# Kernel optimization log

Hardware: AMD Instinct MI355X
Metric: run time of the kernel (lower is better)

Reference implementation:

```python
import jax, jax.numpy as jnp
import numpy as np

NUM_EXPERTS = 8


def setup_inputs() -> dict:
    key = jax.random.key(0)
    k1, k2, k3 = jax.random.split(key, 3)
    M, K, E, N, TOPK = 16384, 1024, NUM_EXPERTS, 2048, 2
    local_hidden_states = jax.random.normal(k1, (M, K), dtype=jnp.float32)
    up_weight = jax.random.normal(k2, (E, K, N), dtype=jnp.float32) * 0.02
    full_topk_ids = jax.random.randint(k3, (M, TOPK), 0, E, dtype=jnp.int64)
    return {
        "local_hidden_states": local_hidden_states,
        "up_weight": up_weight,
        "full_topk_ids": full_topk_ids,
    }


def reference(local_hidden_states, up_weight, full_topk_ids):
    # WORLD_SIZE == 1 -> all-gather is the identity; full token set == local shard.
    full_hidden = local_hidden_states                     # [M, K]
    M, K = full_hidden.shape
    E, _, N = up_weight.shape
    topk = full_topk_ids.shape[1]

    # Each token is routed to `topk` experts: replicate rows, flatten routing ids.
    h_rep = jnp.repeat(full_hidden, topk, axis=0)         # [M*topk, K]
    flat_ids = full_topk_ids.reshape(-1)                  # [M*topk]

    # Expert-grouped GEMM: out[p] = h_rep[p] @ up_weight[flat_ids[p]].
    # Loop over the small fixed expert count, masking rows (dense reference
    # for the irregular grouped GEMM; avoids a [M*topk, K, N] weight gather).
    inter = jnp.zeros((M * topk, N), dtype=full_hidden.dtype)
    for e in range(E):
        mask = (flat_ids == e).astype(full_hidden.dtype)[:, None]   # [M*topk, 1]
        inter = inter + (h_rep @ up_weight[e]) * mask                # [M*topk, N]

    # Fused gated SiLU: split the fused gate/up projection in half.
    half = N // 2
    gate, up = inter[:, :half], inter[:, half:]
    return jax.nn.silu(gate) * up                          # [M*topk, N//2]
```

## Files before the change

kernel.cpp:

```cpp
#include <hip/hip_runtime.h>
#include <hip/hip_bf16.h>
#include <stdint.h>

typedef __attribute__((ext_vector_type(4))) float f32x4;
typedef __attribute__((ext_vector_type(8))) short bf16x8;
typedef __attribute__((ext_vector_type(4))) float float4v;

static constexpr int KD    = 1024;
static constexpr int ND    = 2048;
static constexpr int NE    = 8;
static constexpr int MROWS = 16384;
static constexpr int RFLAT = 32768;
static constexpr int OUTN  = 1024;

static constexpr size_t WS_ROWLIST = 1024;
static constexpr size_t WS_HB      = 262144;
static constexpr size_t WS_WT      = 262144 + (size_t)33554432;

__device__ __forceinline__ unsigned short f2bf(float f) {
  uint32_t u = __float_as_uint(f);
  uint32_t r = (u + 0x7FFFu + ((u >> 16) & 1u)) >> 16;
  return (unsigned short)r;
}

__device__ __forceinline__ void gload16(const void* g, void* l) {
  __builtin_amdgcn_global_load_lds(
      (__attribute__((address_space(1))) void*)(void*)g,
      (__attribute__((address_space(3))) void*)l, 16, 0, 0);
}

__global__ void k_detect(const int* __restrict__ ids32, int* __restrict__ wsi) {
  int t = blockIdx.x * 256 + threadIdx.x;
  int i = 2 * t + 1;
  if (i < RFLAT && ids32[i] != 0) atomicOr(&wsi[31], 1);
}

__device__ __forceinline__ int read_id(const int* ids32, int t, int mode) {
  return (mode ? ids32[t] : ids32[2 * t]) & 7;
}

__global__ void k_count(const int* __restrict__ ids, int* __restrict__ wsi) {
  __shared__ int h[8];
  const int tid = threadIdx.x;
  if (tid < 8) h[tid] = 0;
  __syncthreads();
  const int mode = wsi[31];
  const int base = blockIdx.x * 512 + tid;
  atomicAdd(&h[read_id(ids, base, mode)], 1);
  atomicAdd(&h[read_id(ids, base + 256, mode)], 1);
  __syncthreads();
  if (tid < 8 && h[tid]) atomicAdd(&wsi[tid], h[tid]);
}

__global__ void k_scan(int* wsi) {
  if (threadIdx.x == 0) {
    int o = 0, to = 0;
    for (int e = 0; e < NE; ++e) {
      int c = wsi[e];
      wsi[16 + e] = o;
      wsi[8 + e]  = o;
      wsi[40 + e] = to;
      o += c;
      to += (c + 255) / 256;
    }
    wsi[16 + NE] = o;
    wsi[40 + NE] = to;
  }
}

__global__ void k_scatter(const int* __restrict__ ids, int* __restrict__ wsi,
                          int* __restrict__ rowlist) {
  __shared__ int h[8], base[8], c2[8];
  const int tid = threadIdx.x;
  if (tid < 8) { h[tid] = 0; c2[tid] = 0; }
  __syncthreads();
  const int mode = wsi[31];
  const int t = blockIdx.x * 256 + tid;
  const int e = read_id(ids, t, mode);
  atomicAdd(&h[e], 1);
  __syncthreads();
  if (tid < 8 && h[tid]) base[tid] = atomicAdd(&wsi[8 + tid], h[tid]);
  __syncthreads();
  const int r = atomicAdd(&c2[e], 1);
  rowlist[base[e] + r] = t;
}

__global__ void k_cvtH(const float* __restrict__ H, unsigned short* __restrict__ Hb) {
  const int n4 = (MROWS * KD) / 4;
  const int stride = gridDim.x * blockDim.x;
  for (int i = blockIdx.x * blockDim.x + threadIdx.x; i < n4; i += stride) {
    float4v v = ((const float4v*)H)[i];
    ushort4 o;
    o.x = f2bf(v.x); o.y = f2bf(v.y); o.z = f2bf(v.z); o.w = f2bf(v.w);
    ((ushort4*)Hb)[i] = o;
  }
}

__global__ void k_cvtW(const float* __restrict__ W, unsigned short* __restrict__ Wt) {
  __shared__ float tile[64][65];
  const int e  = blockIdx.z;
  const int n0 = blockIdx.x * 64;
  const int k0 = blockIdx.y * 64;
  const int tx = threadIdx.x, ty = threadIdx.y;
  const float* Wp = W + (size_t)e * KD * ND;
  #pragma unroll
  for (int i = ty; i < 64; i += 8)
    tile[i][tx] = Wp[(size_t)(k0 + i) * ND + n0 + tx];
  __syncthreads();
  unsigned short* Wo = Wt + (size_t)e * ND * KD;
  #pragma unroll
  for (int i = ty; i < 64; i += 8)
    Wo[(size_t)(n0 + i) * KD + k0 + tx] = f2bf(tile[tx][i]);
}

__global__ __launch_bounds__(512, 2) void k_gemm(
    const unsigned short* __restrict__ Hb, const unsigned short* __restrict__ Wt,
    const int* __restrict__ wsi, const int* __restrict__ rowlist,
    float* __restrict__ Out) {
  const int bid = blockIdx.x;
  const int xcd = bid & 7;
  const int j   = bid >> 3;
  const int colblk = j & 7;
  const int rt  = xcd + (j >> 3) * 8;
  if (rt >= wsi[48]) return;
  int e = 0;
  #pragma unroll
  for (int q = 1; q < 8; ++q)
    if (rt >= wsi[40 + q]) e = q;
  const int cnt = wsi[e];
  const int tile_base = (rt - wsi[40 + e]) * 256;
  const int tile_cnt = min(256, cnt - tile_base);
  const int off = wsi[16 + e] + tile_base;
  const int c0 = colblk * 128;

  __shared__ char lds[131072];
  __shared__ int s_rows[256];

  const int t = threadIdx.x;
  if (t < 256) s_rows[t] = rowlist[off + min(t, tile_cnt - 1)];
  __syncthreads();

  const int srow = t >> 2;
  const int coff = ((t & 3) ^ ((t >> 3) & 3)) * 16;
  const char* sA0 = (const char*)Hb + (size_t)(s_rows[srow] >> 1) * (KD * 2) + coff;
  const char* sA1 = (const char*)Hb + (size_t)(s_rows[128 + srow] >> 1) * (KD * 2) + coff;
  auto wcol_of = [&](int jc) {
    const int wn_s = jc >> 6, r64 = jc & 63;
    const int h_s = r64 >> 4, l_s = r64 & 15;
    return (h_s < 2) ? (c0 + wn_s * 32 + h_s * 16 + l_s)
                     : (OUTN + c0 + wn_s * 32 + (h_s - 2) * 16 + l_s);
  };
  const char* sB0 = (const char*)Wt + ((size_t)e * ND + wcol_of(srow)) * (KD * 2) + coff;
  const char* sB1 = (const char*)Wt + ((size_t)e * ND + wcol_of(128 + srow)) * (KD * 2) + coff;

  const int lane = t & 63, wid = t >> 6;
  const int wm = wid >> 2, wn = wid & 3;
  const int kc = lane >> 4, l15 = lane & 15;

  f32x4 acc[8][4];
  #pragma unroll
  for (int m = 0; m < 8; ++m)
    #pragma unroll
    for (int h = 0; h < 4; ++h)
      acc[m][h] = (f32x4){0.f, 0.f, 0.f, 0.f};

  int aoff[8], boff[4];
  #pragma unroll
  for (int m = 0; m < 8; ++m) {
    const int r = wm * 128 + m * 16 + l15;
    aoff[m] = r * 64 + ((kc ^ ((r >> 1) & 3)) * 16);
  }
  #pragma unroll
  for (int h = 0; h < 4; ++h) {
    const int jc = wn * 64 + h * 16 + l15;
    boff[h] = 16384 + jc * 64 + ((kc ^ ((jc >> 1) & 3)) * 16);
  }

  auto SAB = [&](int h, char* slot) {
    const int go = h * 64;
    gload16(sA0 + go, slot + t * 16);
    gload16(sA1 + go, slot + 8192 + t * 16);
    gload16(sB0 + go, slot + 16384 + t * 16);
    gload16(sB1 + go, slot + 24576 + t * 16);
  };

  bf16x8 af[4], bfv[4];
  auto LDA = [&](const char* cb, int mlo) {
    #pragma unroll
    for (int m = 0; m < 4; ++m) af[m] = *(const bf16x8*)(cb + aoff[mlo + m]);
  };
  auto LDB = [&](const char* cb) {
    #pragma unroll
    for (int h = 0; h < 4; ++h) bfv[h] = *(const bf16x8*)(cb + boff[h]);
  };
  auto MM = [&](int mlo) {
    __builtin_amdgcn_s_setprio(1);
    #pragma unroll
    for (int m = 0; m < 4; ++m)
      #pragma unroll
      for (int h = 0; h < 4; ++h)
        acc[mlo + m][h] =
            __builtin_amdgcn_mfma_f32_16x16x32_bf16(af[m], bfv[h], acc[mlo + m][h], 0, 0, 0);
    __builtin_amdgcn_s_setprio(0);
  };
#define GUARD8 asm volatile("s_waitcnt vmcnt(8)" ::: "memory")
#define GUARD4 asm volatile("s_waitcnt vmcnt(4)" ::: "memory")
#define GUARD0 asm volatile("s_waitcnt vmcnt(0)" ::: "memory")
#define BAR __builtin_amdgcn_s_barrier()

  SAB(0, lds);
  SAB(1, lds + 32768);
  SAB(2, lds + 65536);
  GUARD8; BAR;

  for (int k = 0; k < 14; ++k) {
    char* cb0 = lds + (k & 1) * 65536;
    char* cb1 = cb0 + 32768;
    char* st1 = lds + ((k + 1) & 1) * 65536 + 32768;
    LDA(cb0, 0); LDB(cb0);
    SAB(2 * k + 3, st1);
    BAR; MM(0); BAR;
    LDA(cb0, 4);
    GUARD8; BAR; MM(4); BAR;
    LDA(cb1, 0); LDB(cb1);
    SAB(2 * k + 4, cb0);
    BAR; MM(0); BAR;
    LDA(cb1, 4);
    GUARD8; BAR; MM(4); BAR;
  }
  {
    char* cb0 = lds;
    char* cb1 = lds + 32768;
    char* st1 = lds + 98304;
    LDA(cb0, 0); LDB(cb0);
    SAB(31, st1);
    BAR; MM(0); BAR;
    LDA(cb0, 4);
    GUARD8; BAR; MM(4); BAR;
    LDA(cb1, 0); LDB(cb1);
    BAR; MM(0); BAR;
    LDA(cb1, 4);
    GUARD4; BAR; MM(4); BAR;
  }
  {
    char* cb0 = lds + 65536;
    char* cb1 = lds + 98304;
    LDA(cb0, 0); LDB(cb0);
    BAR; MM(0); BAR;
    LDA(cb0, 4);
    GUARD0; BAR; MM(4); BAR;
    LDA(cb1, 0); LDB(cb1);
    BAR; MM(0); BAR;
    LDA(cb1, 4);
    MM(4);
  }
#undef GUARD8
#undef GUARD4
#undef GUARD0
#undef BAR

  #pragma unroll
  for (int m = 0; m < 8; ++m) {
    const int rbase = wm * 128 + m * 16 + kc * 4;
    #pragma unroll
    for (int i = 0; i < 4; ++i) {
      const int rl = rbase + i;
      if (rl < tile_cnt) {
        const size_t orow = (size_t)s_rows[rl] * OUTN;
        #pragma unroll
        for (int h = 0; h < 2; ++h) {
          float gg = acc[m][h][i];
          float uu = acc[m][h + 2][i];
          float s = gg / (1.0f + __expf(-gg)) * uu;
          Out[orow + c0 + wn * 32 + h * 16 + l15] = s;
        }
      }
    }
  }
}

extern "C" void kernel_launch(void* const* d_in, const int* in_sizes, int n_in,
                              void* d_out, int out_size, void* d_ws, size_t ws_size,
                              hipStream_t stream) {
  const float* H  = (const float*)d_in[0];
  const float* W  = (const float*)d_in[1];
  const int* ids  = (const int*)d_in[2];
  float* Out      = (float*)d_out;
  char* ws        = (char*)d_ws;
  int* wsi        = (int*)ws;
  int* rowlist    = (int*)(ws + WS_ROWLIST);
  unsigned short* Hb = (unsigned short*)(ws + WS_HB);
  unsigned short* Wt = (unsigned short*)(ws + WS_WT);

  hipMemsetAsync(ws, 0, 1024, stream);
  k_detect<<<RFLAT / 2 / 256, 256, 0, stream>>>(ids, wsi);
  k_count<<<RFLAT / 512, 256, 0, stream>>>(ids, wsi);
  k_scan<<<1, 64, 0, stream>>>(wsi);
  k_scatter<<<RFLAT / 256, 256, 0, stream>>>(ids, wsi, rowlist);
  k_cvtH<<<2048, 256, 0, stream>>>(H, Hb);
  k_cvtW<<<dim3(ND / 64, KD / 64, NE), dim3(64, 8), 0, stream>>>(W, Wt);
  k_gemm<<<8 * 17 * 8, 512, 0, stream>>>(Hb, Wt, wsi, rowlist, Out);
}
```

Baseline: 233.3 us.

## Halve GEMM column tile to 64, use 256-thread blocks with triple-buffered LDS, vectorize weight transpose

The grouped GEMM now uses 256-row by 64-output-column tiles with 4 waves instead of 8. The LDS ring drops from four 32 KB stages to three 24 KB slots rotated modulo 3, and the grid doubles in column blocks. This lowers LDS use per block to allow more resident blocks and more parallelism, at the cost of re-reading the A rows twice as often. The weight transpose/convert kernel also writes 8 contiguous bf16 values per thread instead of strided scalar stores.

Measured after the change: 228.2 us. 1.02x faster.

```diff
diff --git a/kernel.cpp b/kernel.cpp
--- a/kernel.cpp
+++ b/kernel.cpp
@@ -101,27 +101,33 @@
   const int e  = blockIdx.z;
   const int n0 = blockIdx.x * 64;
   const int k0 = blockIdx.y * 64;
-  const int tx = threadIdx.x, ty = threadIdx.y;
+  const int t  = threadIdx.x;
+  const int tx = t & 63, ty = t >> 6;
   const float* Wp = W + (size_t)e * KD * ND;
   #pragma unroll
   for (int i = ty; i < 64; i += 8)
     tile[i][tx] = Wp[(size_t)(k0 + i) * ND + n0 + tx];
   __syncthreads();
-  unsigned short* Wo = Wt + (size_t)e * ND * KD;
-  #pragma unroll
-  for (int i = ty; i < 64; i += 8)
-    Wo[(size_t)(n0 + i) * KD + k0 + tx] = f2bf(tile[tx][i]);
-}
-
-__global__ __launch_bounds__(512, 2) void k_gemm(
+  const int n = t >> 3, kc8 = (t & 7) * 8;
+  ushort4 o0, o1;
+  o0.x = f2bf(tile[kc8 + 0][n]); o0.y = f2bf(tile[kc8 + 1][n]);
+  o0.z = f2bf(tile[kc8 + 2][n]); o0.w = f2bf(tile[kc8 + 3][n]);
+  o1.x = f2bf(tile[kc8 + 4][n]); o1.y = f2bf(tile[kc8 + 5][n]);
+  o1.z = f2bf(tile[kc8 + 6][n]); o1.w = f2bf(tile[kc8 + 7][n]);
+  unsigned short* Wo = Wt + (size_t)e * ND * KD + (size_t)(n0 + n) * KD + k0 + kc8;
+  *(ushort4*)Wo = o0;
+  *(ushort4*)(Wo + 4) = o1;
+}
+
+__global__ __launch_bounds__(256, 2) void k_gemm(
     const unsigned short* __restrict__ Hb, const unsigned short* __restrict__ Wt,
     const int* __restrict__ wsi, const int* __restrict__ rowlist,
     float* __restrict__ Out) {
   const int bid = blockIdx.x;
   const int xcd = bid & 7;
   const int j   = bid >> 3;
-  const int colblk = j & 7;
-  const int rt  = xcd + (j >> 3) * 8;
+  const int colblk = j & 15;
+  const int rt  = xcd + (j >> 4) * 8;
   if (rt >= wsi[48]) return;
   int e = 0;
   #pragma unroll
@@ -131,30 +137,36 @@
   const int tile_base = (rt - wsi[40 + e]) * 256;
   const int tile_cnt = min(256, cnt - tile_base);
   const int off = wsi[16 + e] + tile_base;
-  const int c0 = colblk * 128;
-
-  __shared__ char lds[131072];
+  const int c0 = colblk * 64;
+
+  constexpr int SLOT = 24576;
+  __shared__ char lds[3 * SLOT];
   __shared__ int s_rows[256];
 
   const int t = threadIdx.x;
-  if (t < 256) s_rows[t] = rowlist[off + min(t, tile_cnt - 1)];
-  __syncthreads();
-
-  const int srow = t >> 2;
+  s_rows[t] = rowlist[off + min(t, tile_cnt - 1)];
+  __syncthreads();
+
   const int coff = ((t & 3) ^ ((t >> 3) & 3)) * 16;
-  const char* sA0 = (const char*)Hb + (size_t)(s_rows[srow] >> 1) * (KD * 2) + coff;
-  const char* sA1 = (const char*)Hb + (size_t)(s_rows[128 + srow] >> 1) * (KD * 2) + coff;
+  const char* srcA[4];
+  const char* srcB[2];
+  #pragma unroll
+  for (int u = 0; u < 4; ++u)
+    srcA[u] = (const char*)Hb +
+              (size_t)(s_rows[u * 64 + (t >> 2)] >> 1) * (KD * 2) + coff;
   auto wcol_of = [&](int jc) {
     const int wn_s = jc >> 6, r64 = jc & 63;
     const int h_s = r64 >> 4, l_s = r64 & 15;
     return (h_s < 2) ? (c0 + wn_s * 32 + h_s * 16 + l_s)
                      : (OUTN + c0 + wn_s * 32 + (h_s - 2) * 16 + l_s);
   };
-  const char* sB0 = (const char*)Wt + ((size_t)e * ND + wcol_of(srow)) * (KD * 2) + coff;
-  const char* sB1 = (const char*)Wt + ((size_t)e * ND + wcol_of(128 + srow)) * (KD * 2) + coff;
+  #pragma unroll
+  for (int u = 0; u < 2; ++u)
+    srcB[u] = (const char*)Wt +
+              ((size_t)e * ND + wcol_of(u * 64 + (t >> 2))) * (KD * 2) + coff;
 
   const int lane = t & 63, wid = t >> 6;
-  const int wm = wid >> 2, wn = wid & 3;
+  const int wm = wid >> 1, wn = wid & 1;
   const int kc = lane >> 4, l15 = lane & 15;
 
   f32x4 acc[8][4];
@@ -178,10 +190,12 @@
 
   auto SAB = [&](int h, char* slot) {
     const int go = h * 64;
-    gload16(sA0 + go, slot + t * 16);
-    gload16(sA1 + go, slot + 8192 + t * 16);
-    gload16(sB0 + go, slot + 16384 + t * 16);
-    gload16(sB1 + go, slot + 24576 + t * 16);
+    gload16(srcA[0] + go, slot + t * 16);
+    gload16(srcA[1] + go, slot + 4096 + t * 16);
+    gload16(srcA[2] + go, slot + 8192 + t * 16);
+    gload16(srcA[3] + go, slot + 12288 + t * 16);
+    gload16(srcB[0] + go, slot + 16384 + t * 16);
+    gload16(srcB[1] + go, slot + 20480 + t * 16);
   };
 
   bf16x8 af[4], bfv[4];
@@ -203,48 +217,32 @@
             __builtin_amdgcn_mfma_f32_16x16x32_bf16(af[m], bfv[h], acc[mlo + m][h], 0, 0, 0);
     __builtin_amdgcn_s_setprio(0);
   };
-#define GUARD8 asm volatile("s_waitcnt vmcnt(8)" ::: "memory")
-#define GUARD4 asm volatile("s_waitcnt vmcnt(4)" ::: "memory")
+#define GUARD6 asm volatile("s_waitcnt vmcnt(6)" ::: "memory")
 #define GUARD0 asm volatile("s_waitcnt vmcnt(0)" ::: "memory")
 #define BAR __builtin_amdgcn_s_barrier()
 
   SAB(0, lds);
-  SAB(1, lds + 32768);
-  SAB(2, lds + 65536);
-  GUARD8; BAR;
-
-  for (int k = 0; k < 14; ++k) {
-    char* cb0 = lds + (k & 1) * 65536;
-    char* cb1 = cb0 + 32768;
-    char* st1 = lds + ((k + 1) & 1) * 65536 + 32768;
+  SAB(1, lds + SLOT);
+  GUARD6; BAR;
+
+  for (int k = 0; k < 15; ++k) {
+    char* cb0 = lds + ((2 * k) % 3) * SLOT;
+    char* cb1 = lds + ((2 * k + 1) % 3) * SLOT;
+    char* st0 = lds + ((2 * k + 2) % 3) * SLOT;
     LDA(cb0, 0); LDB(cb0);
-    SAB(2 * k + 3, st1);
+    SAB(2 * k + 2, st0);
     BAR; MM(0); BAR;
     LDA(cb0, 4);
-    GUARD8; BAR; MM(4); BAR;
+    GUARD6; BAR; MM(4); BAR;
     LDA(cb1, 0); LDB(cb1);
-    SAB(2 * k + 4, cb0);
+    SAB(2 * k + 3, cb0);
     BAR; MM(0); BAR;
     LDA(cb1, 4);
-    GUARD8; BAR; MM(4); BAR;
+    GUARD6; BAR; MM(4); BAR;
   }
   {
     char* cb0 = lds;
-    char* cb1 = lds + 32768;
-    char* st1 = lds + 98304;
-    LDA(cb0, 0); LDB(cb0);
-    SAB(31, st1);
-    BAR; MM(0); BAR;
-    LDA(cb0, 4);
-    GUARD8; BAR; MM(4); BAR;
-    LDA(cb1, 0); LDB(cb1);
-    BAR; MM(0); BAR;
-    LDA(cb1, 4);
-    GUARD4; BAR; MM(4); BAR;
-  }
-  {
-    char* cb0 = lds + 65536;
-    char* cb1 = lds + 98304;
+    char* cb1 = lds + SLOT;
     LDA(cb0, 0); LDB(cb0);
     BAR; MM(0); BAR;
     LDA(cb0, 4);
@@ -254,8 +252,7 @@
     LDA(cb1, 4);
     MM(4);
   }
-#undef GUARD8
-#undef GUARD4
+#undef GUARD6
 #undef GUARD0
 #undef BAR
 
@@ -298,6 +295,6 @@
   k_scan<<<1, 64, 0, stream>>>(wsi);
   k_scatter<<<RFLAT / 256, 256, 0, stream>>>(ids, wsi, rowlist);
   k_cvtH<<<2048, 256, 0, stream>>>(H, Hb);
-  k_cvtW<<<dim3(ND / 64, KD / 64, NE), dim3(64, 8), 0, stream>>>(W, Wt);
-  k_gemm<<<8 * 17 * 8, 512, 0, stream>>>(Hb, Wt, wsi, rowlist, Out);
-}
+  k_cvtW<<<dim3(ND / 64, KD / 64, NE), 512, 0, stream>>>(W, Wt);
+  k_gemm<<<8 * 17 * 16, 256, 0, stream>>>(Hb, Wt, wsi, rowlist, Out);
+}
```
